# Kernel tuning notes

Hardware: AMD Instinct MI355X
Metric: run time of the kernel (lower is better)

Reference implementation:

```python
import math
import jax, jax.numpy as jnp
import numpy as np

B, T, D, V, L, H = 2, 1024, 768, 32768, 4, 12
HD = D // H
STD = 0.02


def layer_norm(x, w, b):
    mu = x.mean(-1, keepdims=True)
    var = ((x - mu) ** 2).mean(-1, keepdims=True)
    return (x - mu) * jax.lax.rsqrt(var + 1e-5) * w + b


def new_gelu(x):
    c = math.sqrt(2.0 / math.pi)
    return 0.5 * x * (1.0 + jnp.tanh(c * (x + 0.044715 * x ** 3)))


def setup_inputs() -> dict:
    key = jax.random.key(0)
    ks = jax.random.split(key, 10)
    idx = jax.random.randint(ks[0], (B, T), 0, V)
    age = jax.random.uniform(ks[1], (B, T), dtype=jnp.float32) * 36500.0  # days
    wte = jax.random.normal(ks[2], (V, D), jnp.float32) * STD  # tied with lm_head
    wae_w = jax.random.normal(ks[3], (D, D), jnp.float32) * STD  # AgeEncoding linear (no bias)
    proj_std = STD / math.sqrt(2 * L)
    return {
        'idx': idx,
        'age': age,
        'wte': wte,
        'wae_w': wae_w,
        'ln1_w': jnp.ones((L, D), jnp.float32),
        'ln1_b': jnp.zeros((L, D), jnp.float32),
        'attn_w': jax.random.normal(ks[4], (L, 3 * D, D), jnp.float32) * STD,
        'attn_b': jnp.zeros((L, 3 * D), jnp.float32),
        'proj_w': jax.random.normal(ks[5], (L, D, D), jnp.float32) * proj_std,
        'proj_b': jnp.zeros((L, D), jnp.float32),
        'ln2_w': jnp.ones((L, D), jnp.float32),
        'ln2_b': jnp.zeros((L, D), jnp.float32),
        'fc_w': jax.random.normal(ks[6], (L, 4 * D, D), jnp.float32) * STD,
        'fc_b': jnp.zeros((L, 4 * D), jnp.float32),
        'fc2_w': jax.random.normal(ks[7], (L, D, 4 * D), jnp.float32) * proj_std,
        'fc2_b': jnp.zeros((L, D), jnp.float32),
        'lnf_w': jnp.ones((D,), jnp.float32),
        'lnf_b': jnp.zeros((D,), jnp.float32),
    }


def _forward(idx, age, wte, wae_w, ln1_w, ln1_b, attn_w, attn_b, proj_w, proj_b,
             ln2_w, ln2_b, fc_w, fc_b, fc2_w, fc2_b, lnf_w, lnf_b):
    # token embedding (tied with lm_head)
    tok = wte[idx]  # [B,T,D]
    # age encoding: interleaved sin/cos of age/365.25 * div_term, then linear
    div = jnp.exp(jnp.arange(0, D, 2).astype(jnp.float32) * (-math.log(10000.0) / D))  # [D/2]
    ang = (age[..., None] / 365.25) * div  # [B,T,D/2]
    y = jnp.zeros((B, T, D), tok.dtype)
    y = y.at[..., 0::2].set(jnp.sin(ang)).at[..., 1::2].set(jnp.cos(ang))
    x = tok + y @ wae_w.T  # token_drop identity at dropout 0 (scaled by 1-0)

    # attention mask: valid-token outer product, causal, plus self-attn for pad tokens
    valid = idx > 0
    tril = jnp.tril(jnp.ones((T, T), bool))
    mask = valid[:, None, None, :] & valid[:, None, :, None] & tril
    mask = (mask | ((~valid)[:, None, None, :] & jnp.eye(T, dtype=bool))) & tril  # [B,1,T,T]

    scale = 1.0 / math.sqrt(HD)

    def block(x, p):
        l1w, l1b, aw, ab, pw, pb, l2w, l2b, fw, fb, f2w, f2b = p
        h = layer_norm(x, l1w, l1b)
        qkv = h @ aw.T + ab
        q, k, v = jnp.split(qkv, 3, axis=-1)
        q = q.reshape(B, T, H, HD).transpose(0, 2, 1, 3)  # [B,H,T,HD]
        k = k.reshape(B, T, H, HD).transpose(0, 2, 1, 3)
        v = v.reshape(B, T, H, HD).transpose(0, 2, 1, 3)
        att = jnp.einsum('bhqd,bhkd->bhqk', q, k) * scale
        att = jnp.where(mask, att, -jnp.inf)
        att = jax.nn.softmax(att, axis=-1)
        yv = jnp.einsum('bhqk,bhkd->bhqd', att, v)
        yv = yv.transpose(0, 2, 1, 3).reshape(B, T, D)
        x = x + yv @ pw.T + pb
        h2 = layer_norm(x, l2w, l2b)
        x = x + new_gelu(h2 @ fw.T + fb) @ f2w.T + f2b
        return x, att

    x, att = jax.lax.scan(block, x, (ln1_w, ln1_b, attn_w, attn_b, proj_w, proj_b,
                                     ln2_w, ln2_b, fc_w, fc_b, fc2_w, fc2_b))
    x = layer_norm(x, lnf_w, lnf_b)
    logits = x @ wte.T  # tied lm_head
    return logits


def reference(idx, age, wte, wae_w, ln1_w, ln1_b, attn_w, attn_b, proj_w, proj_b,
              ln2_w, ln2_b, fc_w, fc_b, fc2_w, fc2_b, lnf_w, lnf_b):
    return _forward(idx, age, wte, wae_w, ln1_w, ln1_b, attn_w, attn_b, proj_w, proj_b,
                    ln2_w, ln2_b, fc_w, fc_b, fc2_w, fc2_b, lnf_w, lnf_b)
```

## Files before the change

### kernel.cpp

```cpp
#include <hip/hip_runtime.h>

typedef unsigned short u16;
typedef __bf16 bf16x8 __attribute__((ext_vector_type(8)));
typedef float f32x4 __attribute__((ext_vector_type(4)));

__device__ __forceinline__ u16 f2bf(float f) {
    union { float f; unsigned int u; } c; c.f = f;
    unsigned int u = c.u;
    unsigned int r = (u + 0x7FFFu + ((u >> 16) & 1u)) >> 16;
    return (u16)r;
}

__device__ __forceinline__ float gelu_f(float v) {
    const float c = 0.7978845608028654f;
    float t = tanhf(c * (v + 0.044715f * v * v * v));
    return 0.5f * v * (1.0f + t);
}

typedef const __attribute__((address_space(1))) unsigned int* as1_u32p;
typedef __attribute__((address_space(3))) unsigned int* as3_u32p;
__device__ __forceinline__ void gload16(const void* g, void* l) {
    __builtin_amdgcn_global_load_lds((as1_u32p)g, (as3_u32p)l, 16, 0, 0);
}

__global__ __launch_bounds__(256) void cvt_kernel(
    const float* __restrict__ src, u16* __restrict__ dst, int n4)
{
    int i = blockIdx.x * 256 + threadIdx.x;
    int stride = gridDim.x * 256;
    for (; i < n4; i += stride) {
        float4 f = reinterpret_cast<const float4*>(src)[i];
        union { u16 h[4]; uint2 u; } cv;
        cv.h[0] = f2bf(f.x); cv.h[1] = f2bf(f.y);
        cv.h[2] = f2bf(f.z); cv.h[3] = f2bf(f.w);
        reinterpret_cast<uint2*>(dst)[i] = cv.u;
    }
}

__global__ __launch_bounds__(256) void embed_kernel(
    const int* __restrict__ idx, const float* __restrict__ age,
    const float* __restrict__ wte, float* __restrict__ x, u16* __restrict__ y)
{
    int t = blockIdx.x;
    int tid = threadIdx.x;
    int tok = idx[t];
    float a = age[t] * (1.0f / 365.25f);
    const float kc = -9.210340371976184f / 768.0f;
#pragma unroll
    for (int j = 0; j < 3; j++) {
        int d = tid + j * 256;
        x[(size_t)t * 768 + d] = wte[(size_t)tok * 768 + d];
        int twoi = d & ~1;
        float dv = __expf(kc * (float)twoi);
        float ang = a * dv;
        float val = (d & 1) ? __cosf(ang) : __sinf(ang);
        y[(size_t)t * 768 + d] = f2bf(val);
    }
}

__global__ __launch_bounds__(256) void ln_kernel(
    const float* __restrict__ x, const float* __restrict__ w,
    const float* __restrict__ b, u16* __restrict__ out)
{
    int row = blockIdx.x;
    int tid = threadIdx.x;
    int l = tid & 63, wv = tid >> 6;
    const float* xr = x + (size_t)row * 768;
    float v[3], s = 0.f, ss = 0.f;
#pragma unroll
    for (int j = 0; j < 3; j++) { v[j] = xr[tid + j * 256]; s += v[j]; ss += v[j] * v[j]; }
#pragma unroll
    for (int d = 1; d < 64; d <<= 1) { s += __shfl_xor(s, d); ss += __shfl_xor(ss, d); }
    __shared__ float ps[4], pss[4];
    if (l == 0) { ps[wv] = s; pss[wv] = ss; }
    __syncthreads();
    s = ps[0] + ps[1] + ps[2] + ps[3];
    ss = pss[0] + pss[1] + pss[2] + pss[3];
    float mu = s * (1.0f / 768.0f);
    float var = ss * (1.0f / 768.0f) - mu * mu;
    float rstd = rsqrtf(var + 1e-5f);
#pragma unroll
    for (int j = 0; j < 3; j++) {
        int d = tid + j * 256;
        out[(size_t)row * 768 + d] = f2bf((v[j] - mu) * rstd * w[d] + b[d]);
    }
}

enum { EPI_BF16 = 0, EPI_BF16_GELU = 1, EPI_F32_RESID = 2, EPI_F32 = 3 };

template <int EPI, int BM, int NWM>
__global__ __launch_bounds__(256) void gemm_db_kernel(
    const u16* __restrict__ A, const u16* __restrict__ B,
    const float* __restrict__ bias, const float* resid, void* out,
    int N, int K, int mtiles, int nwg8)
{
    constexpr int NWN = 4 / NWM;
    constexpr int MI  = (BM / NWM) / 16;
    constexpr int NI  = (128 / NWN) / 16;
    constexpr int ASHOTS = (BM * 4) / 256;
    __shared__ u16 As[2][BM][32];
    __shared__ u16 Bs[2][128][32];
    int tid = threadIdx.x;
    int l = tid & 63, w = tid >> 6;
    int lw = l & 15, lg = l >> 4;
    int bid = blockIdx.x;
    int wg = (bid & 7) * nwg8 + (bid >> 3);
    int mt = wg % mtiles, nt = wg / mtiles;
    int row0 = mt * BM, col0 = nt * 128;
    int wm = w % NWM, wn = w / NWM;
    int mbase = wm * (BM / NWM), nbase = wn * (128 / NWN);

    f32x4 acc[MI][NI] = {};
    const int ntiles = K >> 5;

    auto stage = [&](int nb, int kk) {
        u16* asb = &As[nb][0][0];
        u16* bsb = &Bs[nb][0][0];
#pragma unroll
        for (int s = 0; s < ASHOTS; s++) {
            int c = s * 256 + tid;
            int r = c >> 2, q = (c & 3) * 8;
            gload16(A + (size_t)(row0 + r) * K + kk + q, asb + r * 32 + q);
        }
#pragma unroll
        for (int s = 0; s < 2; s++) {
            int c = s * 256 + tid;
            int r = c >> 2, q = (c & 3) * 8;
            gload16(B + (size_t)(col0 + r) * K + kk + q, bsb + r * 32 + q);
        }
    };

    stage(0, 0);
    __syncthreads();
    for (int t = 0; t < ntiles; ++t) {
        int cur = t & 1;
        if (t + 1 < ntiles) stage(cur ^ 1, (t + 1) << 5);
        bf16x8 af[MI], bfr[NI];
#pragma unroll
        for (int mi = 0; mi < MI; mi++)
            af[mi] = *reinterpret_cast<const bf16x8*>(&As[cur][mbase + mi * 16 + lw][lg * 8]);
#pragma unroll
        for (int ni = 0; ni < NI; ni++)
            bfr[ni] = *reinterpret_cast<const bf16x8*>(&Bs[cur][nbase + ni * 16 + lw][lg * 8]);
        __builtin_amdgcn_s_setprio(1);
#pragma unroll
        for (int mi = 0; mi < MI; mi++)
#pragma unroll
            for (int ni = 0; ni < NI; ni++)
                acc[mi][ni] = __builtin_amdgcn_mfma_f32_16x16x32_bf16(af[mi], bfr[ni], acc[mi][ni], 0, 0, 0);
        __builtin_amdgcn_s_setprio(0);
        __syncthreads();
    }

#pragma unroll
    for (int mi = 0; mi < MI; mi++) {
#pragma unroll
        for (int ni = 0; ni < NI; ni++) {
            int colc = col0 + nbase + ni * 16 + lw;
            float bv = bias ? bias[colc] : 0.0f;
#pragma unroll
            for (int j = 0; j < 4; j++) {
                int row = row0 + mbase + mi * 16 + lg * 4 + j;
                size_t off = (size_t)row * N + colc;
                float v = acc[mi][ni][j] + bv;
                if constexpr (EPI == EPI_BF16) {
                    ((u16*)out)[off] = f2bf(v);
                } else if constexpr (EPI == EPI_BF16_GELU) {
                    ((u16*)out)[off] = f2bf(gelu_f(v));
                } else if constexpr (EPI == EPI_F32_RESID) {
                    ((float*)out)[off] = v + resid[off];
                } else {
                    ((float*)out)[off] = v;
                }
            }
        }
    }
}

template <int EPI>
__global__ __launch_bounds__(256) void gemm_kernel(
    const u16* __restrict__ A, const float* __restrict__ Bw,
    const float* __restrict__ bias, const float* resid, void* out,
    int N, int K)
{
    constexpr int M = 2048;
    __shared__ u16 As[128][40];
    __shared__ u16 Bs[128][40];
    int tid = threadIdx.x;
    int l = tid & 63, w = tid >> 6;
    int lw = l & 15, lg = l >> 4;
    int mtiles = M / 128;
    int mt = blockIdx.x % mtiles, nt = blockIdx.x / mtiles;
    int row0 = mt * 128, col0 = nt * 128;
    int mbase = (w & 1) * 64, nbase = (w >> 1) * 64;
    f32x4 acc[4][4] = {};

    for (int kk = 0; kk < K; kk += 32) {
        int c = tid;
#pragma unroll
        for (int i = 0; i < 2; i++, c += 256) {
            int r = c >> 2, q = c & 3;
            uint4 u = *reinterpret_cast<const uint4*>(A + (size_t)(row0 + r) * K + kk + q * 8);
            *reinterpret_cast<uint4*>(&As[r][q * 8]) = u;
        }
        int c2 = tid;
#pragma unroll
        for (int i = 0; i < 4; i++, c2 += 256) {
            int r = c2 >> 3, q = c2 & 7;
            const float4 f = *reinterpret_cast<const float4*>(Bw + (size_t)(col0 + r) * K + kk + q * 4);
            union { u16 h[4]; uint2 u; } cv;
            cv.h[0] = f2bf(f.x); cv.h[1] = f2bf(f.y); cv.h[2] = f2bf(f.z); cv.h[3] = f2bf(f.w);
            *reinterpret_cast<uint2*>(&Bs[r][q * 4]) = cv.u;
        }
        __syncthreads();
        bf16x8 af[4], bfr[4];
#pragma unroll
        for (int mi = 0; mi < 4; mi++)
            af[mi] = *reinterpret_cast<const bf16x8*>(&As[mbase + mi * 16 + lw][lg * 8]);
#pragma unroll
        for (int ni = 0; ni < 4; ni++)
            bfr[ni] = *reinterpret_cast<const bf16x8*>(&Bs[nbase + ni * 16 + lw][lg * 8]);
#pragma unroll
        for (int mi = 0; mi < 4; mi++)
#pragma unroll
            for (int ni = 0; ni < 4; ni++)
                acc[mi][ni] = __builtin_amdgcn_mfma_f32_16x16x32_bf16(af[mi], bfr[ni], acc[mi][ni], 0, 0, 0);
        __syncthreads();
    }

#pragma unroll
    for (int mi = 0; mi < 4; mi++) {
#pragma unroll
        for (int ni = 0; ni < 4; ni++) {
            int colc = col0 + nbase + ni * 16 + lw;
            float bv = bias ? bias[colc] : 0.0f;
#pragma unroll
            for (int j = 0; j < 4; j++) {
                int row = row0 + mbase + mi * 16 + lg * 4 + j;
                size_t off = (size_t)row * N + colc;
                float v = acc[mi][ni][j] + bv;
                if constexpr (EPI == EPI_BF16) {
                    ((u16*)out)[off] = f2bf(v);
                } else if constexpr (EPI == EPI_BF16_GELU) {
                    ((u16*)out)[off] = f2bf(gelu_f(v));
                } else if constexpr (EPI == EPI_F32_RESID) {
                    ((float*)out)[off] = v + resid[off];
                } else {
                    ((float*)out)[off] = v;
                }
            }
        }
    }
}

__global__ __launch_bounds__(256) void attn_kernel(
    const u16* __restrict__ qkv, const int* __restrict__ idx, u16* __restrict__ yv)
{
    __shared__ u16 Kt[32][72];
    __shared__ u16 Vt[64][40];
    __shared__ u16 Pb[4][16][40];
    __shared__ int kval[32];

    int tid = threadIdx.x, l = tid & 63, w = tid >> 6;
    int lw = l & 15, lg = l >> 4;
    int bid = blockIdx.x;
    int qb = bid & 15;
    int h = (bid >> 4) % 12;
    int b = bid / (16 * 12);
    const size_t base = (size_t)b * 1024;

    int qrow = qb * 64 + w * 16 + lw;
    const u16* qp = qkv + (base + qrow) * 2304 + h * 64;
    bf16x8 aq0 = *reinterpret_cast<const bf16x8*>(qp + lg * 8);
    bf16x8 aq1 = *reinterpret_cast<const bf16x8*>(qp + 32 + lg * 8);

    int rowj[4], vq[4];
#pragma unroll
    for (int j = 0; j < 4; j++) {
        rowj[j] = qb * 64 + w * 16 + lg * 4 + j;
        vq[j] = idx[base + rowj[j]] > 0;
    }
    float m[4], lsum[4];
    f32x4 O[4] = {};
#pragma unroll
    for (int j = 0; j < 4; j++) { m[j] = -__builtin_inff(); lsum[j] = 0.0f; }

    int kvend = qb * 64 + 64;
    for (int kv0 = 0; kv0 < kvend; kv0 += 32) {
        {
            int r = tid >> 3, cc = tid & 7;
            const u16* kp = qkv + (base + kv0 + r) * 2304 + 768 + h * 64 + cc * 8;
            uint4 ku = *reinterpret_cast<const uint4*>(kp);
            *reinterpret_cast<uint4*>(&Kt[r][cc * 8]) = ku;
            const u16* vp = qkv + (base + kv0 + r) * 2304 + 1536 + h * 64 + cc * 8;
            union { uint4 u; u16 h8[8]; } vu;
            vu.u = *reinterpret_cast<const uint4*>(vp);
#pragma unroll
            for (int j2 = 0; j2 < 8; j2++) Vt[cc * 8 + j2][r] = vu.h8[j2];
            if (tid < 32) kval[tid] = idx[base + kv0 + tid] > 0;
        }
        __syncthreads();

        f32x4 S[2];
#pragma unroll
        for (int g = 0; g < 2; g++) {
            bf16x8 bk0 = *reinterpret_cast<const bf16x8*>(&Kt[g * 16 + lw][lg * 8]);
            bf16x8 bk1 = *reinterpret_cast<const bf16x8*>(&Kt[g * 16 + lw][32 + lg * 8]);
            f32x4 t = {};
            t = __builtin_amdgcn_mfma_f32_16x16x32_bf16(aq0, bk0, t, 0, 0, 0);
            t = __builtin_amdgcn_mfma_f32_16x16x32_bf16(aq1, bk1, t, 0, 0, 0);
            S[g] = t;
        }
        float p[2][4];
#pragma unroll
        for (int j = 0; j < 4; j++) {
            float sv0, sv1;
#pragma unroll
            for (int g = 0; g < 2; g++) {
                int kcol = kv0 + g * 16 + lw;
                float s = S[g][j] * 0.125f;
                bool keep = (kcol <= rowj[j]) &&
                            ((vq[j] && kval[g * 16 + lw]) || (kcol == rowj[j]));
                s = keep ? s : -__builtin_inff();
                if (g) sv1 = s; else sv0 = s;
            }
            float mx = fmaxf(sv0, sv1);
            mx = fmaxf(mx, __shfl_xor(mx, 1));
            mx = fmaxf(mx, __shfl_xor(mx, 2));
            mx = fmaxf(mx, __shfl_xor(mx, 4));
            mx = fmaxf(mx, __shfl_xor(mx, 8));
            float mn = fmaxf(m[j], mx);
            float mclamp = fmaxf(mn, -1e30f);
            float scale = __expf(m[j] - mclamp);
            float p0 = __expf(sv0 - mclamp);
            float p1 = __expf(sv1 - mclamp);
            float rs = p0 + p1;
            rs += __shfl_xor(rs, 1); rs += __shfl_xor(rs, 2);
            rs += __shfl_xor(rs, 4); rs += __shfl_xor(rs, 8);
            lsum[j] = lsum[j] * scale + rs;
            m[j] = mn;
#pragma unroll
            for (int ni = 0; ni < 4; ni++) O[ni][j] *= scale;
            p[0][j] = p0; p[1][j] = p1;
        }
#pragma unroll
        for (int g = 0; g < 2; g++)
#pragma unroll
            for (int j = 0; j < 4; j++)
                Pb[w][lg * 4 + j][g * 16 + lw] = f2bf(p[g][j]);
        bf16x8 ap = *reinterpret_cast<const bf16x8*>(&Pb[w][lw][lg * 8]);
#pragma unroll
        for (int ni = 0; ni < 4; ni++) {
            bf16x8 bv = *reinterpret_cast<const bf16x8*>(&Vt[ni * 16 + lw][lg * 8]);
            O[ni] = __builtin_amdgcn_mfma_f32_16x16x32_bf16(ap, bv, O[ni], 0, 0, 0);
        }
        __syncthreads();
    }

#pragma unroll
    for (int j = 0; j < 4; j++) {
        float inv = 1.0f / lsum[j];
#pragma unroll
        for (int ni = 0; ni < 4; ni++) {
            float v = O[ni][j] * inv;
            yv[(base + rowj[j]) * 768 + h * 64 + ni * 16 + lw] = f2bf(v);
        }
    }
}

static void launch_gemm_db(int epi, const u16* A, const u16* B, const float* bias,
                           const float* resid, void* out, int N, int K, hipStream_t s)
{
    dim3 blk(256);
    if (N == 768) {
        constexpr int BM = 64, NWM = 1;
        int mtiles = 2048 / BM;
        int nwg = mtiles * (N / 128);
        dim3 grid(nwg);
        int nwg8 = nwg / 8;
        switch (epi) {
            case EPI_BF16:      gemm_db_kernel<EPI_BF16, BM, NWM><<<grid, blk, 0, s>>>(A, B, bias, resid, out, N, K, mtiles, nwg8); break;
            case EPI_BF16_GELU: gemm_db_kernel<EPI_BF16_GELU, BM, NWM><<<grid, blk, 0, s>>>(A, B, bias, resid, out, N, K, mtiles, nwg8); break;
            case EPI_F32_RESID: gemm_db_kernel<EPI_F32_RESID, BM, NWM><<<grid, blk, 0, s>>>(A, B, bias, resid, out, N, K, mtiles, nwg8); break;
            default:            gemm_db_kernel<EPI_F32, BM, NWM><<<grid, blk, 0, s>>>(A, B, bias, resid, out, N, K, mtiles, nwg8); break;
        }
    } else {
        constexpr int BM = 128, NWM = 2;
        int mtiles = 2048 / BM;
        int nwg = mtiles * (N / 128);
        dim3 grid(nwg);
        int nwg8 = nwg / 8;
        switch (epi) {
            case EPI_BF16:      gemm_db_kernel<EPI_BF16, BM, NWM><<<grid, blk, 0, s>>>(A, B, bias, resid, out, N, K, mtiles, nwg8); break;
            case EPI_BF16_GELU: gemm_db_kernel<EPI_BF16_GELU, BM, NWM><<<grid, blk, 0, s>>>(A, B, bias, resid, out, N, K, mtiles, nwg8); break;
            case EPI_F32_RESID: gemm_db_kernel<EPI_F32_RESID, BM, NWM><<<grid, blk, 0, s>>>(A, B, bias, resid, out, N, K, mtiles, nwg8); break;
            default:            gemm_db_kernel<EPI_F32, BM, NWM><<<grid, blk, 0, s>>>(A, B, bias, resid, out, N, K, mtiles, nwg8); break;
        }
    }
}

static void launch_gemm_f32w(int epi, const u16* A, const float* Bw, const float* bias,
                             const float* resid, void* out, int N, int K, hipStream_t s)
{
    dim3 grid((2048 / 128) * (N / 128)), blk(256);
    switch (epi) {
        case EPI_BF16:      gemm_kernel<EPI_BF16><<<grid, blk, 0, s>>>(A, Bw, bias, resid, out, N, K); break;
        case EPI_BF16_GELU: gemm_kernel<EPI_BF16_GELU><<<grid, blk, 0, s>>>(A, Bw, bias, resid, out, N, K); break;
        case EPI_F32_RESID: gemm_kernel<EPI_F32_RESID><<<grid, blk, 0, s>>>(A, Bw, bias, resid, out, N, K); break;
        default:            gemm_kernel<EPI_F32><<<grid, blk, 0, s>>>(A, Bw, bias, resid, out, N, K); break;
    }
}

static void cvt(const float* src, u16* dst, size_t n, hipStream_t s) {
    int n4 = (int)(n / 4);
    int blocks = (n4 + 255) / 256;
    if (blocks > 2048) blocks = 2048;
    cvt_kernel<<<blocks, 256, 0, s>>>(src, dst, n4);
}

extern "C" void kernel_launch(void* const* d_in, const int* in_sizes, int n_in,
                              void* d_out, int out_size, void* d_ws, size_t ws_size,
                              hipStream_t stream)
{
    (void)in_sizes; (void)n_in; (void)out_size;
    const int*   idx    = (const int*)  d_in[0];
    const float* age    = (const float*)d_in[1];
    const float* wte    = (const float*)d_in[2];
    const float* wae_w  = (const float*)d_in[3];
    const float* ln1_w  = (const float*)d_in[4];
    const float* ln1_b  = (const float*)d_in[5];
    const float* attn_w = (const float*)d_in[6];
    const float* attn_b = (const float*)d_in[7];
    const float* proj_w = (const float*)d_in[8];
    const float* proj_b = (const float*)d_in[9];
    const float* ln2_w  = (const float*)d_in[10];
    const float* ln2_b  = (const float*)d_in[11];
    const float* fc_w   = (const float*)d_in[12];
    const float* fc_b   = (const float*)d_in[13];
    const float* fc2_w  = (const float*)d_in[14];
    const float* fc2_b  = (const float*)d_in[15];
    const float* lnf_w  = (const float*)d_in[16];
    const float* lnf_b  = (const float*)d_in[17];

    char* ws = (char*)d_ws;
    size_t off = 0;
    float* x   = (float*)(ws + off); off += (size_t)2048 * 768 * 4;
    u16* hb    = (u16*)(ws + off);   off += (size_t)2048 * 768 * 2;
    u16* qkvb  = (u16*)(ws + off);   off += (size_t)2048 * 2304 * 2;
    u16* yvb   = (u16*)(ws + off);   off += (size_t)2048 * 768 * 2;
    u16* a1b   = (u16*)(ws + off);   off += (size_t)2048 * 3072 * 2;
    u16* yage  = (u16*)(ws + off);   off += (size_t)2048 * 768 * 2;
    u16* wte_b  = (u16*)(ws + off);  off += (size_t)32768 * 768 * 2;
    u16* attn_wb= (u16*)(ws + off);  off += (size_t)4 * 2304 * 768 * 2;
    u16* proj_wb= (u16*)(ws + off);  off += (size_t)4 * 768 * 768 * 2;
    u16* fc_wb  = (u16*)(ws + off);  off += (size_t)4 * 3072 * 768 * 2;
    u16* fc2_wb = (u16*)(ws + off);  off += (size_t)4 * 768 * 3072 * 2;
    u16* wae_wb = (u16*)(ws + off);  off += (size_t)768 * 768 * 2;
    const size_t NEED = off;

    if (ws_size >= NEED) {
        cvt(wte,    wte_b,   (size_t)32768 * 768, stream);
        cvt(attn_w, attn_wb, (size_t)4 * 2304 * 768, stream);
        cvt(proj_w, proj_wb, (size_t)4 * 768 * 768, stream);
        cvt(fc_w,   fc_wb,   (size_t)4 * 3072 * 768, stream);
        cvt(fc2_w,  fc2_wb,  (size_t)4 * 768 * 3072, stream);
        cvt(wae_w,  wae_wb,  (size_t)768 * 768, stream);

        embed_kernel<<<2048, 256, 0, stream>>>(idx, age, wte, x, yage);
        launch_gemm_db(EPI_F32_RESID, yage, wae_wb, nullptr, x, x, 768, 768, stream);

        for (int li = 0; li < 4; li++) {
            ln_kernel<<<2048, 256, 0, stream>>>(x, ln1_w + li * 768, ln1_b + li * 768, hb);
            launch_gemm_db(EPI_BF16, hb, attn_wb + (size_t)li * 2304 * 768, attn_b + li * 2304,
                           nullptr, qkvb, 2304, 768, stream);
            attn_kernel<<<2 * 12 * 16, 256, 0, stream>>>(qkvb, idx, yvb);
            launch_gemm_db(EPI_F32_RESID, yvb, proj_wb + (size_t)li * 768 * 768, proj_b + li * 768,
                           x, x, 768, 768, stream);
            ln_kernel<<<2048, 256, 0, stream>>>(x, ln2_w + li * 768, ln2_b + li * 768, hb);
            launch_gemm_db(EPI_BF16_GELU, hb, fc_wb + (size_t)li * 3072 * 768, fc_b + li * 3072,
                           nullptr, a1b, 3072, 768, stream);
            launch_gemm_db(EPI_F32_RESID, a1b, fc2_wb + (size_t)li * 768 * 3072, fc2_b + li * 768,
                           x, x, 768, 3072, stream);
        }

        ln_kernel<<<2048, 256, 0, stream>>>(x, lnf_w, lnf_b, hb);
        launch_gemm_db(EPI_F32, hb, wte_b, nullptr, nullptr, d_out, 32768, 768, stream);
    } else {
        embed_kernel<<<2048, 256, 0, stream>>>(idx, age, wte, x, yage);
        launch_gemm_f32w(EPI_F32_RESID, yage, wae_w, nullptr, x, x, 768, 768, stream);
        for (int li = 0; li < 4; li++) {
            ln_kernel<<<2048, 256, 0, stream>>>(x, ln1_w + li * 768, ln1_b + li * 768, hb);
            launch_gemm_f32w(EPI_BF16, hb, attn_w + (size_t)li * 2304 * 768, attn_b + li * 2304,
                             nullptr, qkvb, 2304, 768, stream);
            attn_kernel<<<2 * 12 * 16, 256, 0, stream>>>(qkvb, idx, yvb);
            launch_gemm_f32w(EPI_F32_RESID, yvb, proj_w + (size_t)li * 768 * 768, proj_b + li * 768,
                             x, x, 768, 768, stream);
            ln_kernel<<<2048, 256, 0, stream>>>(x, ln2_w + li * 768, ln2_b + li * 768, hb);
            launch_gemm_f32w(EPI_BF16_GELU, hb, fc_w + (size_t)li * 3072 * 768, fc_b + li * 3072,
                             nullptr, a1b, 3072, 768, stream);
            launch_gemm_f32w(EPI_F32_RESID, a1b, fc2_w + (size_t)li * 768 * 3072, fc2_b + li * 768,
                             x, x, 768, 3072, stream);
        }
        ln_kernel<<<2048, 256, 0, stream>>>(x, lnf_w, lnf_b, hb);
        launch_gemm_f32w(EPI_F32, hb, wte, nullptr, nullptr, d_out, 32768, 768, stream);
    }
}
```

Measured before the change: 1.553 ms.

## Deepen GEMM global-to-LDS pipeline to four stages with explicit vmcnt waits

```diff
diff --git a/kernel.cpp b/kernel.cpp
--- a/kernel.cpp
+++ b/kernel.cpp
@@ -21,6 +21,14 @@
 typedef __attribute__((address_space(3))) unsigned int* as3_u32p;
 __device__ __forceinline__ void gload16(const void* g, void* l) {
     __builtin_amdgcn_global_load_lds((as1_u32p)g, (as3_u32p)l, 16, 0, 0);
+}
+
+template <int N> __device__ __forceinline__ void wait_vmcnt() {
+    if constexpr (N == 0)      asm volatile("s_waitcnt vmcnt(0)" ::: "memory");
+    else if constexpr (N == 3) asm volatile("s_waitcnt vmcnt(3)" ::: "memory");
+    else if constexpr (N == 4) asm volatile("s_waitcnt vmcnt(4)" ::: "memory");
+    else if constexpr (N == 6) asm volatile("s_waitcnt vmcnt(6)" ::: "memory");
+    else if constexpr (N == 8) asm volatile("s_waitcnt vmcnt(8)" ::: "memory");
 }
 
 __global__ __launch_bounds__(256) void cvt_kernel(
@@ -89,7 +97,7 @@
 enum { EPI_BF16 = 0, EPI_BF16_GELU = 1, EPI_F32_RESID = 2, EPI_F32 = 3 };
 
 template <int EPI, int BM, int NWM>
-__global__ __launch_bounds__(256) void gemm_db_kernel(
+__global__ __launch_bounds__(256) void gemm_p3_kernel(
     const u16* __restrict__ A, const u16* __restrict__ B,
     const float* __restrict__ bias, const float* resid, void* out,
     int N, int K, int mtiles, int nwg8)
@@ -98,8 +106,9 @@
     constexpr int MI  = (BM / NWM) / 16;
     constexpr int NI  = (128 / NWN) / 16;
     constexpr int ASHOTS = (BM * 4) / 256;
-    __shared__ u16 As[2][BM][32];
-    __shared__ u16 Bs[2][128][32];
+    constexpr int LPS = ASHOTS + 2;
+    __shared__ u16 As[4][BM][32];
+    __shared__ u16 Bs[4][128][32];
     int tid = threadIdx.x;
     int l = tid & 63, w = tid >> 6;
     int lw = l & 15, lg = l >> 4;
@@ -131,10 +140,13 @@
     };
 
     stage(0, 0);
-    __syncthreads();
+    stage(1, 32);
+    stage(2, 64);
+    wait_vmcnt<2 * LPS>();
+    __builtin_amdgcn_s_barrier();
+
     for (int t = 0; t < ntiles; ++t) {
-        int cur = t & 1;
-        if (t + 1 < ntiles) stage(cur ^ 1, (t + 1) << 5);
+        int cur = t & 3;
         bf16x8 af[MI], bfr[NI];
 #pragma unroll
         for (int mi = 0; mi < MI; mi++)
@@ -142,6 +154,7 @@
 #pragma unroll
         for (int ni = 0; ni < NI; ni++)
             bfr[ni] = *reinterpret_cast<const bf16x8*>(&Bs[cur][nbase + ni * 16 + lw][lg * 8]);
+        if (t + 3 < ntiles) stage((t + 3) & 3, (t + 3) << 5);
         __builtin_amdgcn_s_setprio(1);
 #pragma unroll
         for (int mi = 0; mi < MI; mi++)
@@ -149,7 +162,11 @@
             for (int ni = 0; ni < NI; ni++)
                 acc[mi][ni] = __builtin_amdgcn_mfma_f32_16x16x32_bf16(af[mi], bfr[ni], acc[mi][ni], 0, 0, 0);
         __builtin_amdgcn_s_setprio(0);
-        __syncthreads();
+        int rem = ntiles - 1 - t;
+        if (rem >= 3)      wait_vmcnt<2 * LPS>();
+        else if (rem == 2) wait_vmcnt<LPS>();
+        else if (rem == 1) wait_vmcnt<0>();
+        __builtin_amdgcn_s_barrier();
     }
 
 #pragma unroll
@@ -379,10 +396,10 @@
         dim3 grid(nwg);
         int nwg8 = nwg / 8;
         switch (epi) {
-            case EPI_BF16:      gemm_db_kernel<EPI_BF16, BM, NWM><<<grid, blk, 0, s>>>(A, B, bias, resid, out, N, K, mtiles, nwg8); break;
-            case EPI_BF16_GELU: gemm_db_kernel<EPI_BF16_GELU, BM, NWM><<<grid, blk, 0, s>>>(A, B, bias, resid, out, N, K, mtiles, nwg8); break;
-            case EPI_F32_RESID: gemm_db_kernel<EPI_F32_RESID, BM, NWM><<<grid, blk, 0, s>>>(A, B, bias, resid, out, N, K, mtiles, nwg8); break;
-            default:            gemm_db_kernel<EPI_F32, BM, NWM><<<grid, blk, 0, s>>>(A, B, bias, resid, out, N, K, mtiles, nwg8); break;
+            case EPI_BF16:      gemm_p3_kernel<EPI_BF16, BM, NWM><<<grid, blk, 0, s>>>(A, B, bias, resid, out, N, K, mtiles, nwg8); break;
+            case EPI_BF16_GELU: gemm_p3_kernel<EPI_BF16_GELU, BM, NWM><<<grid, blk, 0, s>>>(A, B, bias, resid, out, N, K, mtiles, nwg8); break;
+            case EPI_F32_RESID: gemm_p3_kernel<EPI_F32_RESID, BM, NWM><<<grid, blk, 0, s>>>(A, B, bias, resid, out, N, K, mtiles, nwg8); break;
+            default:            gemm_p3_kernel<EPI_F32, BM, NWM><<<grid, blk, 0, s>>>(A, B, bias, resid, out, N, K, mtiles, nwg8); break;
         }
     } else {
         constexpr int BM = 128, NWM = 2;
@@ -391,10 +408,10 @@
         dim3 grid(nwg);
         int nwg8 = nwg / 8;
         switch (epi) {
-            case EPI_BF16:      gemm_db_kernel<EPI_BF16, BM, NWM><<<grid, blk, 0, s>>>(A, B, bias, resid, out, N, K, mtiles, nwg8); break;
-            case EPI_BF16_GELU: gemm_db_kernel<EPI_BF16_GELU, BM, NWM><<<grid, blk, 0, s>>>(A, B, bias, resid, out, N, K, mtiles, nwg8); break;
-            case EPI_F32_RESID: gemm_db_kernel<EPI_F32_RESID, BM, NWM><<<grid, blk, 0, s>>>(A, B, bias, resid, out, N, K, mtiles, nwg8); break;
-            default:            gemm_db_kernel<EPI_F32, BM, NWM><<<grid, blk, 0, s>>>(A, B, bias, resid, out, N, K, mtiles, nwg8); break;
+            case EPI_BF16:      gemm_p3_kernel<EPI_BF16, BM, NWM><<<grid, blk, 0, s>>>(A, B, bias, resid, out, N, K, mtiles, nwg8); break;
+            case EPI_BF16_GELU: gemm_p3_kernel<EPI_BF16_GELU, BM, NWM><<<grid, blk, 0, s>>>(A, B, bias, resid, out, N, K, mtiles, nwg8); break;
+            case EPI_F32_RESID: gemm_p3_kernel<EPI_F32_RESID, BM, NWM><<<grid, blk, 0, s>>>(A, B, bias, resid, out, N, K, mtiles, nwg8); break;
+            default:            gemm_p3_kernel<EPI_F32, BM, NWM><<<grid, blk, 0, s>>>(A, B, bias, resid, out, N, K, mtiles, nwg8); break;
         }
     }
 }
```

Measured after the change: 1.552 ms. Within noise of the previous version (-0.1%).
